# Kernel optimization log

Hardware: AMD Instinct MI355X
Metric: run time of the kernel (lower is better)

Reference implementation:

```python
import jax, jax.numpy as jnp
import numpy as np

N = 100000   # nodes
E = 1000000  # edges
IN = 100     # input feature dim
H = 4        # heads
D = 32       # hidden per head (H*D = 128)
C = 47       # classes
EPS = 1e-5
SLOPE = 0.2  # DGL GATv2 leaky_relu negative slope


def setup_inputs() -> dict:
    key = jax.random.key(0)
    ks = jax.random.split(key, 32)
    lin = lambda k, i, o: (jax.random.normal(k, (i, o), jnp.float32) / np.float32(np.sqrt(i)))
    inp = {}
    inp['x'] = jax.random.normal(ks[0], (N, IN), jnp.float32)
    inp['src'] = jax.random.randint(ks[1], (E,), 0, N, jnp.int32)
    inp['dst'] = jnp.sort(jax.random.randint(ks[2], (E,), 0, N, jnp.int32))
    # layer 0: IN -> H*D, Linear residual (IN != H*D)
    inp['Wsrc0'] = lin(ks[3], IN, H * D); inp['bsrc0'] = jnp.zeros(H * D, jnp.float32)
    inp['Wdst0'] = lin(ks[4], IN, H * D); inp['bdst0'] = jnp.zeros(H * D, jnp.float32)
    inp['attn0'] = lin(ks[5], H, D)
    inp['Wres0'] = lin(ks[6], IN, H * D); inp['bres0'] = jnp.zeros(H * D, jnp.float32)
    # layer 1: H*D -> H*D, Identity residual (128 == 128)
    inp['Wsrc1'] = lin(ks[7], H * D, H * D); inp['bsrc1'] = jnp.zeros(H * D, jnp.float32)
    inp['Wdst1'] = lin(ks[8], H * D, H * D); inp['bdst1'] = jnp.zeros(H * D, jnp.float32)
    inp['attn1'] = lin(ks[9], H, D)
    # layer 2: H*D -> H*C, Linear residual (128 != 188)
    inp['Wsrc2'] = lin(ks[10], H * D, H * C); inp['bsrc2'] = jnp.zeros(H * C, jnp.float32)
    inp['Wdst2'] = lin(ks[11], H * D, H * C); inp['bdst2'] = jnp.zeros(H * C, jnp.float32)
    inp['attn2'] = lin(ks[12], H, C)
    inp['Wres2'] = lin(ks[13], H * D, H * C); inp['bres2'] = jnp.zeros(H * C, jnp.float32)
    # BatchNorm1d params (training-mode batch stats)
    inp['g0'] = jnp.ones(H * D, jnp.float32); inp['be0'] = jnp.zeros(H * D, jnp.float32)
    inp['g1'] = jnp.ones(H * D, jnp.float32); inp['be1'] = jnp.zeros(H * D, jnp.float32)
    return inp


def _gatv2(h, src, dst, Ws, bs, Wd, bd, attn, resval):
    """One GATv2Conv on a full block (src feats == dst feats == h)."""
    Hh, Dd = attn.shape
    fs = (h @ Ws + bs).reshape(-1, Hh, Dd)   # [N,H,D] src projection
    fd = (h @ Wd + bd).reshape(-1, Hh, Dd)   # [N,H,D] dst projection
    e = jax.nn.leaky_relu(fs[src] + fd[dst], SLOPE)         # [E,H,D]
    logits = jnp.einsum('ehd,hd->eh', e, attn)              # [E,H]
    m = jax.ops.segment_max(logits, dst, num_segments=N)    # per-dst max
    ex = jnp.exp(logits - m[dst])
    s = jax.ops.segment_sum(ex, dst, num_segments=N)
    alpha = ex / s[dst]                                      # edge softmax
    out = jax.ops.segment_sum(alpha[:, :, None] * fs[src], dst, num_segments=N)
    return out + resval                                      # [N,H,D]


def _bn(x, g, b):
    mu = x.mean(0)
    v = x.var(0)  # biased, as torch BN training mode
    return g * (x - mu) / jnp.sqrt(v + EPS) + b


def reference(x, src, dst,
              Wsrc0, bsrc0, Wdst0, bdst0, attn0, Wres0, bres0,
              Wsrc1, bsrc1, Wdst1, bdst1, attn1,
              Wsrc2, bsrc2, Wdst2, bdst2, attn2, Wres2, bres2,
              g0, be0, g1, be1):
    # layer 0: conv(+relu activation) -> flatten -> BN -> relu (dropout = eval identity)
    res0 = (x @ Wres0 + bres0).reshape(N, H, D)
    h = jax.nn.relu(_gatv2(x, src, dst, Wsrc0, bsrc0, Wdst0, bdst0, attn0, res0))
    h = jax.nn.relu(_bn(h.reshape(N, H * D), g0, be0))
    # layer 1: Identity residual
    res1 = h.reshape(N, H, D)
    h = jax.nn.relu(_gatv2(h, src, dst, Wsrc1, bsrc1, Wdst1, bdst1, attn1, res1))
    h = jax.nn.relu(_bn(h.reshape(N, H * D), g1, be1))
    # layer 2: no activation; mean over heads; log_softmax
    res2 = (h @ Wres2 + bres2).reshape(N, H, C)
    h = _gatv2(h, src, dst, Wsrc2, bsrc2, Wdst2, bdst2, attn2, res2)
    h = h.mean(1)                                # [N,C]
    return jax.nn.log_softmax(h, axis=-1)
```

## Files before the change

kernel.cpp:

```cpp
#include <hip/hip_runtime.h>
#include <hip/hip_bf16.h>

#define Nn 100000
#define Ee 1000000
#define INF_ 100
#define Hh 4
#define Dd 32
#define HD 128
#define Cc 47
#define HC 188
#define HCP 192
#define EPSV 1e-5f
#define SLOPE 0.2f
#define NBLK ((Nn + 255) / 256)

typedef __hip_bfloat16 bf16;
typedef __attribute__((ext_vector_type(8))) short short8;
typedef __attribute__((ext_vector_type(4))) float f32x4;
typedef __attribute__((ext_vector_type(2))) float f32x2;

__device__ __forceinline__ float tof(bf16 v) { return __bfloat162float(v); }
__device__ __forceinline__ float b2f(unsigned short u) {
    return __uint_as_float((unsigned)u << 16);
}
__device__ __forceinline__ float ldb(const bf16* p) {
    return b2f(*(const unsigned short*)p);
}
__device__ __forceinline__ unsigned short f2u(float v) {
    bf16 t = __float2bfloat16(v);
    return *(unsigned short*)&t;
}
__device__ __forceinline__ f32x2 pk2(float x, float y) {
    f32x2 r; r.x = x; r.y = y; return r;
}
__device__ __forceinline__ f32x2 pabs2(f32x2 v) {
    return __builtin_elementwise_max(v, -v);
}
__device__ __forceinline__ f32x2 pfma2(f32x2 a, f32x2 b, f32x2 c) {
    return __builtin_elementwise_fma(a, b, c);
}

template <int C>
__device__ __forceinline__ float dppadd(float v) {
    int m = __builtin_amdgcn_update_dpp(0, __float_as_int(v), C, 0xF, 0xF, false);
    return v + __int_as_float(m);
}
template <int C>
__device__ __forceinline__ float dppmax(float v) {
    int m = __builtin_amdgcn_update_dpp(0, __float_as_int(v), C, 0xF, 0xF, false);
    return fmaxf(v, __int_as_float(m));
}
__device__ __forceinline__ float sum16(float p) {
    p = dppadd<0xB1>(p);
    p = dppadd<0x4E>(p);
    p = dppadd<0x124>(p);
    p = dppadd<0x128>(p);
    return p;
}
__device__ __forceinline__ float max16(float p) {
    p = dppmax<0xB1>(p); p = dppmax<0x4E>(p);
    p = dppmax<0x124>(p); p = dppmax<0x128>(p);
    return p;
}

#define L2E 1.4426950408889634f
#define LN2 0.6931471805599453f

__global__ void detect_dtype(const unsigned* __restrict__ x, int* __restrict__ flag) {
    if (blockIdx.x == 0 && threadIdx.x == 0) {
        int good = 0;
        for (int i = 0; i < 256; ++i) {
            unsigned lo = x[i] & 0xFFFFu;
            float v = __uint_as_float(lo << 16);
            float a = fabsf(v);
            if (a > 1e-4f && a < 10.f) good++;
        }
        *flag = (good >= 128) ? 1 : 0;
    }
}

__device__ __forceinline__ float ld_any(const void* p, int i, int isbf) {
    return isbf ? tof(((const bf16*)p)[i]) : ((const float*)p)[i];
}

__global__ void cvt_x(const void* __restrict__ in, bf16* __restrict__ out,
                      const int* __restrict__ flag) {
    int i = blockIdx.x * blockDim.x + threadIdx.x;
    if (i >= Nn * 128) return;
    int row = i >> 7, col = i & 127;
    float v = (col < INF_) ? ld_any(in, row * INF_ + col, *flag) : 0.f;
    out[i] = __float2bfloat16(v);
}

#define WROWS 1280
#define NSP 15
struct PrepTab { const void* src[8]; int row0[8]; int K[8]; int M[8]; int MP[8]; };
struct CvtTab { const void* src[NSP]; int off[NSP + 1]; };

__global__ void prep_all(PrepTab t, CvtTab ct, bf16* __restrict__ wtb,
                         bf16* __restrict__ pb, int total,
                         const int* __restrict__ flag) {
    int i = blockIdx.x * blockDim.x + threadIdx.x;
    int isbf = *flag;
    if (i < WROWS * 128) {
        int row = i >> 7, k = i & 127;
        float v = 0.f;
#pragma unroll
        for (int q = 0; q < 8; ++q) {
            if (row >= t.row0[q] && row < t.row0[q] + t.MP[q]) {
                int m = row - t.row0[q];
                if (m < t.M[q] && k < t.K[q])
                    v = ld_any(t.src[q], k * t.M[q] + m, isbf);
            }
        }
        wtb[i] = __float2bfloat16(v);
    }
    if (i < total) {
        int seg = 0;
        while (i >= ct.off[seg + 1]) seg++;
        pb[i] = __float2bfloat16(ld_any(ct.src[seg], i - ct.off[seg], isbf));
    }
}

__global__ void src_scale_ptr(const int* __restrict__ src, const int* __restrict__ dst,
                              unsigned* __restrict__ w384, unsigned* __restrict__ w256,
                              int* __restrict__ ptr,
                              float* __restrict__ z0, float* __restrict__ z1) {
    int i = blockIdx.x * blockDim.x + threadIdx.x;
    if (i < Ee) {
        unsigned s = (unsigned)src[i];
        w384[i] = s * 384u;
        w256[i] = s << 8;
    }
    if (i < 2 * HD) { z0[i] = 0.f; z1[i] = 0.f; }
    if (i <= Nn) {
        if (i == Nn) { ptr[Nn] = Ee; return; }
        int lo = 0, hi = Ee;
        while (lo < hi) {
            int mid = (lo + hi) >> 1;
            if (dst[mid] < i) lo = mid + 1; else hi = mid;
        }
        ptr[i] = lo;
    }
}

__global__ void deg_hist_blk(const int* __restrict__ ptr, int* __restrict__ cnt) {
    __shared__ int lh[256];
    int t = threadIdx.x;
    lh[t] = 0;
    __syncthreads();
    int n = blockIdx.x * 256 + t;
    if (n < Nn) {
        int dg = ptr[n + 1] - ptr[n]; if (dg > 255) dg = 255;
        atomicAdd(&lh[dg], 1);
    }
    __syncthreads();
    cnt[t * NBLK + blockIdx.x] = lh[t];
}

__global__ void deg_totals(const int* __restrict__ cnt, int* __restrict__ totals) {
    int wave = threadIdx.x >> 6, lane = threadIdx.x & 63;
    int bin = blockIdx.x * 4 + wave;
    int s = 0;
    for (int k = lane; k < NBLK; k += 64) s += cnt[bin * NBLK + k];
#pragma unroll
    for (int o = 1; o < 64; o <<= 1) s += __shfl_xor(s, o);
    if (lane == 0) totals[bin] = s;
}

__global__ void deg_bases(const int* __restrict__ cnt, const int* __restrict__ totals,
                          int* __restrict__ base) {
    int wave = threadIdx.x >> 6, lane = threadIdx.x & 63;
    int bin = blockIdx.x * 4 + wave;
    int bb = 0;
    for (int b = bin + 1 + lane; b < 256; b += 64) bb += totals[b];
#pragma unroll
    for (int o = 1; o < 64; o <<= 1) bb += __shfl_xor(bb, o);
    int run = bb;
    for (int k0 = 0; k0 < NBLK; k0 += 64) {
        int k = k0 + lane;
        int c = (k < NBLK) ? cnt[bin * NBLK + k] : 0;
        int p = c;
#pragma unroll
        for (int o = 1; o < 64; o <<= 1) {
            int t = __shfl_up(p, o);
            if (lane >= o) p += t;
        }
        if (k < NBLK) base[bin * NBLK + k] = run + (p - c);
        run += __shfl(p, 63);
    }
}

__global__ void deg_scatter_blk(const int* __restrict__ ptr, const int* __restrict__ base,
                                int* __restrict__ perm) {
    __shared__ int lh[256];
    int t = threadIdx.x;
    lh[t] = 0;
    __syncthreads();
    int n = blockIdx.x * 256 + t;
    if (n < Nn) {
        int dg = ptr[n + 1] - ptr[n]; if (dg > 255) dg = 255;
        int loc = atomicAdd(&lh[dg], 1);
        perm[base[dg * NBLK + blockIdx.x] + loc] = n;
    }
}

template <int MP, int NOUT, int CS, bool ABN, bool PAD47, int OSTR>
__global__ __launch_bounds__(256, 4) void gemm_big(
    const bf16* __restrict__ A, const bf16* __restrict__ Wt,
    const bf16* __restrict__ b0, const bf16* __restrict__ b1,
    const bf16* __restrict__ b2,
    bf16* __restrict__ o0, bf16* __restrict__ o1, bf16* __restrict__ o2,
    int MR, const float* __restrict__ bnp) {
    constexpr int CS64 = CS * 64;
    constexpr int PITCH = CS64 + 8;
    constexpr int LSZ = (64 * PITCH > 64 * 136) ? 64 * PITCH : 64 * 136;
    __shared__ __align__(16) bf16 Al[LSZ];
    const int row0 = blockIdx.x * 64;
    const int tid = threadIdx.x;
#pragma unroll
    for (int j = 0; j < 4; ++j) {
        int idx = tid + j * 256;
        int r = idx >> 4, kk = (idx & 15) * 8;
        int4 val = {0, 0, 0, 0};
        if (row0 + r < Nn) {
            val = *(const int4*)&A[(size_t)(row0 + r) * 128 + kk];
            if (ABN) {
                short8 av = *(short8*)&val;
                bf16 tmp[8];
#pragma unroll
                for (int u = 0; u < 8; ++u) {
                    float v = b2f((unsigned short)av[u]);
                    v = fmaxf(fmaf(v, bnp[kk + u], bnp[128 + kk + u]), 0.f);
                    tmp[u] = __float2bfloat16(v);
                }
                val = *(int4*)tmp;
            }
        }
        *(int4*)&Al[r * 136 + kk] = val;
    }
    __syncthreads();
    const int wave = tid >> 6, lane = tid & 63;
    const int n16 = lane & 15, quad = lane >> 4;
    const int colbase = blockIdx.y * CS64 + wave * (16 * CS);
    f32x4 acc[4][CS];
#pragma unroll
    for (int rt = 0; rt < 4; ++rt)
#pragma unroll
        for (int c = 0; c < CS; ++c) acc[rt][c] = (f32x4){0.f, 0.f, 0.f, 0.f};
    const bf16* wb[CS];
#pragma unroll
    for (int c = 0; c < CS; ++c)
        wb[c] = Wt + (size_t)(colbase + c * 16 + n16) * 128 + quad * 8;
    const bf16* ap = Al + n16 * 136 + quad * 8;
#pragma unroll
    for (int ks = 0; ks < 4; ++ks) {
        short8 bf[CS];
#pragma unroll
        for (int c = 0; c < CS; ++c) bf[c] = *(const short8*)(wb[c] + ks * 32);
#pragma unroll
        for (int rt = 0; rt < 4; ++rt) {
            short8 af = *(const short8*)(ap + rt * 16 * 136 + ks * 32);
#pragma unroll
            for (int c = 0; c < CS; ++c)
                acc[rt][c] = __builtin_amdgcn_mfma_f32_16x16x32_bf16(af, bf[c], acc[rt][c], 0, 0, 0);
        }
    }
    __syncthreads();
    if (PAD47) {
        for (int z = tid; z < 64 * PITCH; z += 256) Al[z] = __float2bfloat16(0.f);
        __syncthreads();
    }
#pragma unroll
    for (int c = 0; c < CS; ++c) {
        int pos = wave * (16 * CS) + c * 16 + n16;
        int col = colbase + c * 16 + n16;
        int oi = col / MP, lc = col - oi * MP;
        bool valid = (oi < NOUT) && (lc < MR);
        float bb = 0.f;
        if (valid) {
            const bf16* bp = (oi == 0) ? b0 : (oi == 1) ? b1 : b2;
            bb = tof(bp[lc]);
        }
        int stp = PAD47 ? (lc + lc / 47) : pos;
#pragma unroll
        for (int rt = 0; rt < 4; ++rt) {
#pragma unroll
            for (int i = 0; i < 4; ++i) {
                int rl = rt * 16 + quad * 4 + i;
                if (valid) Al[rl * PITCH + stp] = __float2bfloat16(acc[rt][c][i] + bb);
            }
        }
    }
    __syncthreads();
    constexpr int NG = CS64 / 8;
    for (int t = tid; t < 64 * NG; t += 256) {
        int rl = t / NG, g = t % NG;
        int row = row0 + rl;
        if (row >= Nn) continue;
        int pos0 = g * 8;
        int oi, lc0;
        if (PAD47) { oi = blockIdx.y; lc0 = pos0; }
        else {
            int col0 = blockIdx.y * CS64 + pos0;
            oi = col0 / MP; lc0 = col0 - oi * MP;
        }
        if (oi >= NOUT) continue;
        bf16* o = (oi == 0) ? o0 : (oi == 1) ? o1 : o2;
        int4 v = *(int4*)&Al[rl * PITCH + pos0];
        *(int4*)&o[(size_t)row * OSTR + lc0] = v;
    }
}

template <bool RESBN>
__global__ __launch_bounds__(256) void gat_fused_128(
    const bf16* __restrict__ fs, const bf16* __restrict__ fd,
    const unsigned* __restrict__ srcW, const int* __restrict__ ptr,
    const int* __restrict__ perm,
    const bf16* __restrict__ attn, const bf16* __restrict__ resb,
    const float* __restrict__ bnp, bf16* __restrict__ hout) {
    const int wave = threadIdx.x >> 6, lane = threadIdx.x & 63;
    const int di = blockIdx.x * 4 + wave;
    if (di >= Nn) return;
    const int d = perm[di];
    const int c0 = lane * 2;
    const unsigned c0b = (unsigned)c0 * 2u;
    ushort2 aq = *(const ushort2*)&attn[c0];
    float a0 = b2f(aq.x) * L2E, a1 = b2f(aq.y) * L2E;
    const f32x2 Av = pk2(0.6f * a0, 0.6f * a1);
    const f32x2 Bv = pk2(0.4f * a0, 0.4f * a1);
    ushort2 dq = *(const ushort2*)&fd[(size_t)d * HD + c0];
    const f32x2 fdv = pk2(b2f(dq.x), b2f(dq.y));
    const char* fsb = (const char*)fs;
    float l = 0.f;
    f32x2 Ov = pk2(0.f, 0.f);
    int e = ptr[d];
    const int e1 = ptr[d + 1];
    for (; e < e1 && (e & 3); ++e) {
        unsigned v = srcW[e] + c0b;
        ushort2 fq = *(const ushort2*)(fsb + v);
        f32x2 f = pk2(b2f(fq.x), b2f(fq.y));
        f32x2 x = f + fdv;
        f32x2 t = pfma2(pabs2(x), Bv, x * Av);
        float p = sum16(t.x + t.y);
        float pe = __builtin_amdgcn_exp2f(p);
        l += pe;
        Ov = pfma2(pk2(pe, pe), f, Ov);
    }
    for (; e + 3 < e1; e += 4) {
        uint4 sw = *(const uint4*)&srcW[e];
        unsigned vA = sw.x + c0b, vB = sw.y + c0b;
        unsigned vC = sw.z + c0b, vD = sw.w + c0b;
        ushort2 qA = *(const ushort2*)(fsb + vA);
        ushort2 qB = *(const ushort2*)(fsb + vB);
        ushort2 qC = *(const ushort2*)(fsb + vC);
        ushort2 qD = *(const ushort2*)(fsb + vD);
        f32x2 fA = pk2(b2f(qA.x), b2f(qA.y));
        f32x2 fB = pk2(b2f(qB.x), b2f(qB.y));
        f32x2 fC = pk2(b2f(qC.x), b2f(qC.y));
        f32x2 fD = pk2(b2f(qD.x), b2f(qD.y));
        f32x2 xA = fA + fdv, xB = fB + fdv, xC = fC + fdv, xD = fD + fdv;
        f32x2 tA = pfma2(pabs2(xA), Bv, xA * Av);
        f32x2 tB = pfma2(pabs2(xB), Bv, xB * Av);
        f32x2 tC = pfma2(pabs2(xC), Bv, xC * Av);
        f32x2 tD = pfma2(pabs2(xD), Bv, xD * Av);
        float pA = tA.x + tA.y, pB = tB.x + tB.y;
        float pC = tC.x + tC.y, pD = tD.x + tD.y;
        pA = sum16(pA); pB = sum16(pB); pC = sum16(pC); pD = sum16(pD);
        float eA = __builtin_amdgcn_exp2f(pA), eB = __builtin_amdgcn_exp2f(pB);
        float eC = __builtin_amdgcn_exp2f(pC), eD = __builtin_amdgcn_exp2f(pD);
        l += (eA + eB) + (eC + eD);
        Ov = pfma2(pk2(eA, eA), fA, Ov);
        Ov = pfma2(pk2(eB, eB), fB, Ov);
        Ov = pfma2(pk2(eC, eC), fC, Ov);
        Ov = pfma2(pk2(eD, eD), fD, Ov);
    }
    for (; e < e1; ++e) {
        unsigned v = srcW[e] + c0b;
        ushort2 fq = *(const ushort2*)(fsb + v);
        f32x2 f = pk2(b2f(fq.x), b2f(fq.y));
        f32x2 x = f + fdv;
        f32x2 t = pfma2(pabs2(x), Bv, x * Av);
        float p = sum16(t.x + t.y);
        float pe = __builtin_amdgcn_exp2f(p);
        l += pe;
        Ov = pfma2(pk2(pe, pe), f, Ov);
    }
    float inv = l > 0.f ? 1.f / l : 0.f;
    ushort2 rq = *(const ushort2*)&resb[(size_t)d * HD + c0];
    float r0 = b2f(rq.x), r1 = b2f(rq.y);
    if (RESBN) {
        r0 = fmaxf(fmaf(r0, bnp[c0], bnp[HD + c0]), 0.f);
        r1 = fmaxf(fmaf(r1, bnp[c0 + 1], bnp[HD + c0 + 1]), 0.f);
    }
    float v0 = fmaxf(fmaf(Ov.x, inv, r0), 0.f);
    float v1 = fmaxf(fmaf(Ov.y, inv, r1), 0.f);
    ushort2 ov; ov.x = f2u(v0); ov.y = f2u(v1);
    *(ushort2*)&hout[(size_t)d * HD + c0] = ov;
}

__global__ __launch_bounds__(256) void gat_fused_188(
    const bf16* __restrict__ fs, const bf16* __restrict__ fd,
    const unsigned* __restrict__ srcW, const int* __restrict__ ptr,
    const int* __restrict__ perm,
    const bf16* __restrict__ attn, const bf16* __restrict__ rs,
    void* __restrict__ out, const int* __restrict__ flag) {
    const int wave = threadIdx.x >> 6, lane = threadIdx.x & 63;
    const int di = blockIdx.x * 4 + wave;
    if (di >= Nn) return;
    const int d = perm[di];
    const int h = lane >> 4, j = lane & 15;
    const int c0 = h * 48 + j;
    const unsigned c0b = (unsigned)c0 * 2u;
    const int ca = h * Cc + j;
    const bool has2 = (j < 15);
    float a0 = ldb(&attn[ca]) * L2E;
    float a1 = ldb(&attn[ca + 16]) * L2E;
    float a2 = has2 ? ldb(&attn[ca + 32]) * L2E : 0.f;
    float A0 = 0.6f * a0, B0 = 0.4f * a0;
    float A1 = 0.6f * a1, B1 = 0.4f * a1;
    float A2 = 0.6f * a2, B2 = 0.4f * a2;
    const bf16* fdr = fd + (size_t)d * HCP;
    float fd0 = ldb(&fdr[c0]);
    float fd1 = ldb(&fdr[c0 + 16]);
    float fd2 = ldb(&fdr[c0 + 32]);
    const char* fsb = (const char*)fs;
    float l = 0.f, O0 = 0.f, O1 = 0.f, O2 = 0.f;
    int e = ptr[d];
    const int e1 = ptr[d + 1];
    for (; e + 3 < e1; e += 4) {
        unsigned vA = srcW[e] + c0b, vB = srcW[e + 1] + c0b;
        unsigned vC = srcW[e + 2] + c0b, vD = srcW[e + 3] + c0b;
        float fA0 = b2f(*(const unsigned short*)(fsb + vA));
        float fA1 = b2f(*(const unsigned short*)(fsb + vA + 32));
        float fA2 = b2f(*(const unsigned short*)(fsb + vA + 64));
        float fB0 = b2f(*(const unsigned short*)(fsb + vB));
        float fB1 = b2f(*(const unsigned short*)(fsb + vB + 32));
        float fB2 = b2f(*(const unsigned short*)(fsb + vB + 64));
        float fC0 = b2f(*(const unsigned short*)(fsb + vC));
        float fC1 = b2f(*(const unsigned short*)(fsb + vC + 32));
        float fC2 = b2f(*(const unsigned short*)(fsb + vC + 64));
        float fD0 = b2f(*(const unsigned short*)(fsb + vD));
        float fD1 = b2f(*(const unsigned short*)(fsb + vD + 32));
        float fD2 = b2f(*(const unsigned short*)(fsb + vD + 64));
        float xA0 = fA0 + fd0, xA1 = fA1 + fd1, xA2 = fA2 + fd2;
        float xB0 = fB0 + fd0, xB1 = fB1 + fd1, xB2 = fB2 + fd2;
        float xC0 = fC0 + fd0, xC1 = fC1 + fd1, xC2 = fC2 + fd2;
        float xD0 = fD0 + fd0, xD1 = fD1 + fd1, xD2 = fD2 + fd2;
        float pA = fmaf(xA0, A0, fmaf(fabsf(xA0), B0, fmaf(xA1, A1, fmaf(fabsf(xA1), B1,
                   fmaf(xA2, A2, fabsf(xA2) * B2)))));
        float pB = fmaf(xB0, A0, fmaf(fabsf(xB0), B0, fmaf(xB1, A1, fmaf(fabsf(xB1), B1,
                   fmaf(xB2, A2, fabsf(xB2) * B2)))));
        float pC = fmaf(xC0, A0, fmaf(fabsf(xC0), B0, fmaf(xC1, A1, fmaf(fabsf(xC1), B1,
                   fmaf(xC2, A2, fabsf(xC2) * B2)))));
        float pD = fmaf(xD0, A0, fmaf(fabsf(xD0), B0, fmaf(xD1, A1, fmaf(fabsf(xD1), B1,
                   fmaf(xD2, A2, fabsf(xD2) * B2)))));
        pA = sum16(pA); pB = sum16(pB); pC = sum16(pC); pD = sum16(pD);
        float eA = __builtin_amdgcn_exp2f(pA), eB = __builtin_amdgcn_exp2f(pB);
        float eC = __builtin_amdgcn_exp2f(pC), eD = __builtin_amdgcn_exp2f(pD);
        l += (eA + eB) + (eC + eD);
        O0 = fmaf(eA, fA0, O0); O0 = fmaf(eB, fB0, O0);
        O0 = fmaf(eC, fC0, O0); O0 = fmaf(eD, fD0, O0);
        O1 = fmaf(eA, fA1, O1); O1 = fmaf(eB, fB1, O1);
        O1 = fmaf(eC, fC1, O1); O1 = fmaf(eD, fD1, O1);
        O2 = fmaf(eA, fA2, O2); O2 = fmaf(eB, fB2, O2);
        O2 = fmaf(eC, fC2, O2); O2 = fmaf(eD, fD2, O2);
    }
    for (; e < e1; ++e) {
        unsigned v = srcW[e] + c0b;
        float f0 = b2f(*(const unsigned short*)(fsb + v));
        float f1 = b2f(*(const unsigned short*)(fsb + v + 32));
        float f2 = b2f(*(const unsigned short*)(fsb + v + 64));
        float x0 = f0 + fd0, x1 = f1 + fd1, x2 = f2 + fd2;
        float p = fmaf(x0, A0, fmaf(fabsf(x0), B0, fmaf(x1, A1, fmaf(fabsf(x1), B1,
                  fmaf(x2, A2, fabsf(x2) * B2)))));
        p = sum16(p);
        float pe = __builtin_amdgcn_exp2f(p);
        l += pe;
        O0 = fmaf(pe, f0, O0);
        O1 = fmaf(pe, f1, O1);
        O2 = fmaf(pe, f2, O2);
    }
    float inv = l > 0.f ? 1.f / l : 0.f;
    const bf16* rr = rs + (size_t)d * HCP;
    float v0 = fmaf(O0, inv, ldb(&rr[c0]));
    float v1 = fmaf(O1, inv, ldb(&rr[c0 + 16]));
    float v2 = has2 ? fmaf(O2, inv, ldb(&rr[c0 + 32])) : 0.f;
    v0 += __shfl_xor(v0, 16); v0 += __shfl_xor(v0, 32); v0 *= 0.25f;
    v1 += __shfl_xor(v1, 16); v1 += __shfl_xor(v1, 32); v1 *= 0.25f;
    v2 += __shfl_xor(v2, 16); v2 += __shfl_xor(v2, 32); v2 *= 0.25f;
    float mx = fmaxf(v0, v1);
    if (has2) mx = fmaxf(mx, v2);
    mx = max16(mx);
    float sm = __expf(v0 - mx) + __expf(v1 - mx) + (has2 ? __expf(v2 - mx) : 0.f);
    sm = sum16(sm);
    if (h == 0) {
        float ls = mx + __log2f(sm) * LN2;
        if (*flag) {
            bf16* o = (bf16*)out + (size_t)d * Cc;
            o[j] = __float2bfloat16(v0 - ls);
            o[j + 16] = __float2bfloat16(v1 - ls);
            if (has2) o[j + 32] = __float2bfloat16(v2 - ls);
        } else {
            float* o = (float*)out + (size_t)d * Cc;
            o[j] = v0 - ls;
            o[j + 16] = v1 - ls;
            if (has2) o[j + 32] = v2 - ls;
        }
    }
}

__global__ void col_stats(const bf16* __restrict__ in, float* __restrict__ sums) {
    int c = threadIdx.x;
    int r0 = blockIdx.x * 256;
    int r1 = r0 + 256; if (r1 > Nn) r1 = Nn;
    float s = 0.f, s2 = 0.f;
    for (int r = r0; r < r1; ++r) {
        float v = ldb(&in[(size_t)r * HD + c]);
        s += v; s2 += v * v;
    }
    atomicAdd(&sums[c], s);
    atomicAdd(&sums[HD + c], s2);
}

__global__ void bn_finalize(const float* __restrict__ sums, const bf16* __restrict__ g,
                            const bf16* __restrict__ be, float* __restrict__ ss) {
    int c = threadIdx.x;
    float mu = sums[c] * (1.f / Nn);
    float var = sums[HD + c] * (1.f / Nn) - mu * mu;
    float sc = tof(g[c]) * rsqrtf(var + EPSV);
    ss[c] = sc;
    ss[HD + c] = tof(be[c]) - mu * sc;
}

extern "C" void kernel_launch(void* const* d_in, const int* in_sizes, int n_in,
                              void* d_out, int out_size, void* d_ws, size_t ws_size,
                              hipStream_t stream) {
    (void)in_sizes; (void)n_in; (void)out_size; (void)ws_size;
    const void* x = d_in[0];
    const int* src = (const int*)d_in[1];
    const int* dst = (const int*)d_in[2];

    char* ws = (char*)d_ws;
    size_t off = 0;
    auto alloc = [&](size_t bytes) {
        void* p = ws + off;
        off += (bytes + 255) & ~(size_t)255;
        return p;
    };
    bf16* xb = (bf16*)alloc((size_t)Nn * 128 * 2);
    bf16* rb = (bf16*)alloc((size_t)Nn * HD * 2);
    bf16* rs = xb;
    bf16* fs = (bf16*)alloc((size_t)Nn * HCP * 2);
    bf16* fd = (bf16*)alloc((size_t)Nn * HCP * 2);
    bf16* hbA = (bf16*)alloc((size_t)Nn * HD * 2);
    bf16* hbB = (bf16*)alloc((size_t)Nn * HD * 2);
    int* ptr = (int*)alloc((Nn + 1) * 4);
    bf16* wtb = (bf16*)alloc((size_t)WROWS * 128 * 2);
    float* bns0 = (float*)alloc(2 * HD * 4);
    float* bns1 = (float*)alloc(2 * HD * 4);
    float* bnss0 = (float*)alloc(2 * HD * 4);
    float* bnss1 = (float*)alloc(2 * HD * 4);
    bf16* pb = (bf16*)alloc(4096 * 2);
    int* flag = (int*)alloc(256);
    unsigned* w384 = (unsigned*)alloc((size_t)Ee * 4);
    unsigned* w256 = (unsigned*)alloc((size_t)Ee * 4);
    int* cnt = (int*)alloc((size_t)256 * NBLK * 4);
    int* cbase = (int*)alloc((size_t)256 * NBLK * 4);
    int* totals = (int*)alloc(256 * 4);
    int* perm = (int*)alloc((size_t)Nn * 4);

    static const int spIdx[NSP] = {4, 6, 7, 9, 11, 13, 14, 16, 18, 19, 21, 22, 23, 24, 25};
    static const int spSz[NSP]  = {HD, HD, HD, HD, HD, HD, HD, HC, HC, HC, HC, HD, HD, HD, HD};
    CvtTab tab;
    int tot = 0;
    for (int i = 0; i < NSP; ++i) { tab.src[i] = d_in[spIdx[i]]; tab.off[i] = tot; tot += spSz[i]; }
    tab.off[NSP] = tot;
    const bf16 *bsrc0 = pb + tab.off[0], *bdst0 = pb + tab.off[1], *attn0 = pb + tab.off[2],
               *bres0 = pb + tab.off[3], *bsrc1 = pb + tab.off[4], *bdst1 = pb + tab.off[5],
               *attn1 = pb + tab.off[6], *bsrc2 = pb + tab.off[7], *bdst2 = pb + tab.off[8],
               *attn2 = pb + tab.off[9], *bres2 = pb + tab.off[10],
               *g0 = pb + tab.off[11], *be0 = pb + tab.off[12],
               *g1 = pb + tab.off[13], *be1 = pb + tab.off[14];

    PrepTab pt;
    static const int wIdx[8] = {3, 5, 8, 10, 12, 15, 17, 20};
    static const int wK[8]   = {INF_, INF_, INF_, HD, HD, HD, HD, HD};
    static const int wM[8]   = {HD, HD, HD, HD, HD, HC, HC, HC};
    static const int wMP[8]  = {128, 128, 128, 128, 128, 192, 192, 192};
    static const int wR0[8]  = {0, 128, 256, 384, 512, 640, 832, 1024};
    for (int i = 0; i < 8; ++i) {
        pt.src[i] = d_in[wIdx[i]]; pt.row0[i] = wR0[i];
        pt.K[i] = wK[i]; pt.M[i] = wM[i]; pt.MP[i] = wMP[i];
    }

    detect_dtype<<<1, 64, 0, stream>>>((const unsigned*)x, flag);
    cvt_x<<<(Nn * 128 + 255) / 256, 256, 0, stream>>>(x, xb, flag);
    prep_all<<<(WROWS * 128 + 255) / 256, 256, 0, stream>>>(pt, tab, wtb, pb, tot, flag);
    src_scale_ptr<<<(Ee + 255) / 256, 256, 0, stream>>>(src, dst, w384, w256, ptr,
                                                        bns0, bns1);
    deg_hist_blk<<<NBLK, 256, 0, stream>>>(ptr, cnt);
    deg_totals<<<64, 256, 0, stream>>>(cnt, totals);
    deg_bases<<<64, 256, 0, stream>>>(cnt, totals, cbase);
    deg_scatter_blk<<<NBLK, 256, 0, stream>>>(ptr, cbase, perm);

    const int fusedGrid = (Nn + 3) / 4;
    const int statsGrid = NBLK;
    const int rowBlk = (Nn + 63) / 64;

    gemm_big<128, 3, 3, false, false, HD><<<dim3(rowBlk, 2), 256, 0, stream>>>(
        xb, wtb, bsrc0, bdst0, bres0, fs, fd, rb, HD, nullptr);
    gat_fused_128<false><<<fusedGrid, 256, 0, stream>>>(fs, fd, w256, ptr, perm,
                                                        attn0, rb, nullptr, hbA);
    col_stats<<<statsGrid, 128, 0, stream>>>(hbA, bns0);
    bn_finalize<<<1, HD, 0, stream>>>(bns0, g0, be0, bnss0);

    gemm_big<128, 2, 2, true, false, HD><<<dim3(rowBlk, 2), 256, 0, stream>>>(
        hbA, wtb + (size_t)384 * 128, bsrc1, bdst1, nullptr, fs, fd, nullptr, HD, bnss0);
    gat_fused_128<true><<<fusedGrid, 256, 0, stream>>>(fs, fd, w256, ptr, perm,
                                                       attn1, hbA, bnss0, hbB);
    col_stats<<<statsGrid, 128, 0, stream>>>(hbB, bns1);
    bn_finalize<<<1, HD, 0, stream>>>(bns1, g1, be1, bnss1);

    gemm_big<192, 3, 3, true, true, HCP><<<dim3(rowBlk, 3), 256, 0, stream>>>(
        hbB, wtb + (size_t)640 * 128, bsrc2, bdst2, bres2, fs, fd, rs, HC, bnss1);
    gat_fused_188<<<fusedGrid, 256, 0, stream>>>(fs, fd, w384, ptr, perm, attn2, rs,
                                                 d_out, flag);
}
```

Baseline: 663.7 us.

## Fuse preprocessing kernels into one launch and fold BN finalize into consumers

Merges the dtype detection, x conversion, weight/param prep, source scaling, CSR pointer search and degree histogram into a single prepare kernel. Each block re-detects the dtype with a ballot, and the degree histogram reads CSR bounds from shared memory instead of a separate pass. The two bn_finalize launches are removed: the GEMM and gat_fused kernels compute the BN scale and offset from the raw sums themselves. This cuts about six launches and their gaps, at the cost of redundant per-thread BN math and a larger grid doing mixed work.

```diff
diff --git a/kernel.cpp b/kernel.cpp
--- a/kernel.cpp
+++ b/kernel.cpp
@@ -66,30 +66,17 @@
 #define L2E 1.4426950408889634f
 #define LN2 0.6931471805599453f
 
-__global__ void detect_dtype(const unsigned* __restrict__ x, int* __restrict__ flag) {
-    if (blockIdx.x == 0 && threadIdx.x == 0) {
-        int good = 0;
-        for (int i = 0; i < 256; ++i) {
-            unsigned lo = x[i] & 0xFFFFu;
-            float v = __uint_as_float(lo << 16);
-            float a = fabsf(v);
-            if (a > 1e-4f && a < 10.f) good++;
-        }
-        *flag = (good >= 128) ? 1 : 0;
-    }
-}
-
 __device__ __forceinline__ float ld_any(const void* p, int i, int isbf) {
     return isbf ? tof(((const bf16*)p)[i]) : ((const float*)p)[i];
 }
 
-__global__ void cvt_x(const void* __restrict__ in, bf16* __restrict__ out,
-                      const int* __restrict__ flag) {
-    int i = blockIdx.x * blockDim.x + threadIdx.x;
-    if (i >= Nn * 128) return;
-    int row = i >> 7, col = i & 127;
-    float v = (col < INF_) ? ld_any(in, row * INF_ + col, *flag) : 0.f;
-    out[i] = __float2bfloat16(v);
+__device__ __forceinline__ int lbound(const int* __restrict__ dst, int n) {
+    int lo = 0, hi = Ee;
+    while (lo < hi) {
+        int mid = (lo + hi) >> 1;
+        if (dst[mid] < n) lo = mid + 1; else hi = mid;
+    }
+    return lo;
 }
 
 #define WROWS 1280
@@ -97,65 +84,72 @@
 struct PrepTab { const void* src[8]; int row0[8]; int K[8]; int M[8]; int MP[8]; };
 struct CvtTab { const void* src[NSP]; int off[NSP + 1]; };
 
-__global__ void prep_all(PrepTab t, CvtTab ct, bf16* __restrict__ wtb,
-                         bf16* __restrict__ pb, int total,
-                         const int* __restrict__ flag) {
-    int i = blockIdx.x * blockDim.x + threadIdx.x;
-    int isbf = *flag;
-    if (i < WROWS * 128) {
-        int row = i >> 7, k = i & 127;
+__global__ __launch_bounds__(256) void prepare(
+    const void* __restrict__ x, const int* __restrict__ src,
+    const int* __restrict__ dst,
+    PrepTab pt, CvtTab ct, int tot,
+    bf16* __restrict__ xb, bf16* __restrict__ wtb, bf16* __restrict__ pb,
+    unsigned* __restrict__ w384, unsigned* __restrict__ w256,
+    int* __restrict__ ptr, int* __restrict__ cnt,
+    float* __restrict__ z0, float* __restrict__ z1, int* __restrict__ flag) {
+    __shared__ int wc[4];
+    __shared__ int lbv[257];
+    __shared__ int lh[256];
+    const int t = threadIdx.x;
+    unsigned w = ((const unsigned*)x)[t];
+    float dv = __uint_as_float((w & 0xFFFFu) << 16);
+    float da = fabsf(dv);
+    unsigned long long m = __ballot(da > 1e-4f && da < 10.f);
+    if ((t & 63) == 0) wc[t >> 6] = __popcll(m);
+    __syncthreads();
+    const int isbf = (wc[0] + wc[1] + wc[2] + wc[3]) >= 128;
+    if (blockIdx.x == 0 && t == 0) *flag = isbf;
+
+    const int gi = blockIdx.x * 256 + t;
+    if (gi < Nn * 128) {
+        int row = gi >> 7, col = gi & 127;
+        float v = (col < INF_) ? ld_any(x, row * INF_ + col, isbf) : 0.f;
+        xb[gi] = __float2bfloat16(v);
+    }
+    if (gi < WROWS * 128) {
+        int row = gi >> 7, k = gi & 127;
         float v = 0.f;
 #pragma unroll
         for (int q = 0; q < 8; ++q) {
-            if (row >= t.row0[q] && row < t.row0[q] + t.MP[q]) {
-                int m = row - t.row0[q];
-                if (m < t.M[q] && k < t.K[q])
-                    v = ld_any(t.src[q], k * t.M[q] + m, isbf);
+            if (row >= pt.row0[q] && row < pt.row0[q] + pt.MP[q]) {
+                int mm = row - pt.row0[q];
+                if (mm < pt.M[q] && k < pt.K[q])
+                    v = ld_any(pt.src[q], k * pt.M[q] + mm, isbf);
             }
         }
-        wtb[i] = __float2bfloat16(v);
-    }
-    if (i < total) {
+        wtb[gi] = __float2bfloat16(v);
+    }
+    if (gi < tot) {
         int seg = 0;
-        while (i >= ct.off[seg + 1]) seg++;
-        pb[i] = __float2bfloat16(ld_any(ct.src[seg], i - ct.off[seg], isbf));
-    }
-}
-
-__global__ void src_scale_ptr(const int* __restrict__ src, const int* __restrict__ dst,
-                              unsigned* __restrict__ w384, unsigned* __restrict__ w256,
-                              int* __restrict__ ptr,
-                              float* __restrict__ z0, float* __restrict__ z1) {
-    int i = blockIdx.x * blockDim.x + threadIdx.x;
-    if (i < Ee) {
-        unsigned s = (unsigned)src[i];
-        w384[i] = s * 384u;
-        w256[i] = s << 8;
-    }
-    if (i < 2 * HD) { z0[i] = 0.f; z1[i] = 0.f; }
-    if (i <= Nn) {
-        if (i == Nn) { ptr[Nn] = Ee; return; }
-        int lo = 0, hi = Ee;
-        while (lo < hi) {
-            int mid = (lo + hi) >> 1;
-            if (dst[mid] < i) lo = mid + 1; else hi = mid;
-        }
-        ptr[i] = lo;
-    }
-}
-
-__global__ void deg_hist_blk(const int* __restrict__ ptr, int* __restrict__ cnt) {
-    __shared__ int lh[256];
-    int t = threadIdx.x;
-    lh[t] = 0;
-    __syncthreads();
-    int n = blockIdx.x * 256 + t;
-    if (n < Nn) {
-        int dg = ptr[n + 1] - ptr[n]; if (dg > 255) dg = 255;
-        atomicAdd(&lh[dg], 1);
-    }
-    __syncthreads();
-    cnt[t * NBLK + blockIdx.x] = lh[t];
+        while (gi >= ct.off[seg + 1]) seg++;
+        pb[gi] = __float2bfloat16(ld_any(ct.src[seg], gi - ct.off[seg], isbf));
+    }
+    if (gi < Ee) {
+        unsigned s = (unsigned)src[gi];
+        w384[gi] = s * 384u;
+        w256[gi] = s << 8;
+    }
+    if (gi < 2 * HD) { z0[gi] = 0.f; z1[gi] = 0.f; }
+    if (blockIdx.x < NBLK) {
+        int nn = gi;
+        int lb = Ee;
+        if (nn <= Nn) { lb = lbound(dst, nn); ptr[nn] = lb; }
+        lbv[t] = lb;
+        if (t == 255) lbv[256] = (nn + 1 <= Nn) ? lbound(dst, nn + 1) : Ee;
+        lh[t] = 0;
+        __syncthreads();
+        if (nn < Nn) {
+            int dg = lbv[t + 1] - lbv[t]; if (dg > 255) dg = 255;
+            atomicAdd(&lh[dg], 1);
+        }
+        __syncthreads();
+        cnt[t * NBLK + blockIdx.x] = lh[t];
+    }
 }
 
 __global__ void deg_totals(const int* __restrict__ cnt, int* __restrict__ totals) {
@@ -211,13 +205,25 @@
     const bf16* __restrict__ b0, const bf16* __restrict__ b1,
     const bf16* __restrict__ b2,
     bf16* __restrict__ o0, bf16* __restrict__ o1, bf16* __restrict__ o2,
-    int MR, const float* __restrict__ bnp) {
+    int MR, const float* __restrict__ sums,
+    const bf16* __restrict__ gg, const bf16* __restrict__ bbn) {
     constexpr int CS64 = CS * 64;
     constexpr int PITCH = CS64 + 8;
     constexpr int LSZ = (64 * PITCH > 64 * 136) ? 64 * PITCH : 64 * 136;
     __shared__ __align__(16) bf16 Al[LSZ];
+    __shared__ float scb[ABN ? HD : 1], ofb[ABN ? HD : 1];
     const int row0 = blockIdx.x * 64;
     const int tid = threadIdx.x;
+    if (ABN) {
+        if (tid < HD) {
+            float mu = sums[tid] * (1.f / Nn);
+            float var = sums[HD + tid] * (1.f / Nn) - mu * mu;
+            float sc = tof(gg[tid]) * rsqrtf(var + EPSV);
+            scb[tid] = sc;
+            ofb[tid] = tof(bbn[tid]) - mu * sc;
+        }
+        __syncthreads();
+    }
 #pragma unroll
     for (int j = 0; j < 4; ++j) {
         int idx = tid + j * 256;
@@ -231,7 +237,7 @@
 #pragma unroll
                 for (int u = 0; u < 8; ++u) {
                     float v = b2f((unsigned short)av[u]);
-                    v = fmaxf(fmaf(v, bnp[kk + u], bnp[128 + kk + u]), 0.f);
+                    v = fmaxf(fmaf(v, scb[kk + u], ofb[kk + u]), 0.f);
                     tmp[u] = __float2bfloat16(v);
                 }
                 val = *(int4*)tmp;
@@ -318,7 +324,8 @@
     const unsigned* __restrict__ srcW, const int* __restrict__ ptr,
     const int* __restrict__ perm,
     const bf16* __restrict__ attn, const bf16* __restrict__ resb,
-    const float* __restrict__ bnp, bf16* __restrict__ hout) {
+    const float* __restrict__ sums, const bf16* __restrict__ gv,
+    const bf16* __restrict__ bev, bf16* __restrict__ hout) {
     const int wave = threadIdx.x >> 6, lane = threadIdx.x & 63;
     const int di = blockIdx.x * 4 + wave;
     if (di >= Nn) return;
@@ -390,8 +397,15 @@
     ushort2 rq = *(const ushort2*)&resb[(size_t)d * HD + c0];
     float r0 = b2f(rq.x), r1 = b2f(rq.y);
     if (RESBN) {
-        r0 = fmaxf(fmaf(r0, bnp[c0], bnp[HD + c0]), 0.f);
-        r1 = fmaxf(fmaf(r1, bnp[c0 + 1], bnp[HD + c0 + 1]), 0.f);
+        float mu0 = sums[c0] * (1.f / Nn), mu1 = sums[c0 + 1] * (1.f / Nn);
+        float va0 = sums[HD + c0] * (1.f / Nn) - mu0 * mu0;
+        float va1 = sums[HD + c0 + 1] * (1.f / Nn) - mu1 * mu1;
+        float sc0 = tof(gv[c0]) * rsqrtf(va0 + EPSV);
+        float sc1 = tof(gv[c0 + 1]) * rsqrtf(va1 + EPSV);
+        float of0 = tof(bev[c0]) - mu0 * sc0;
+        float of1 = tof(bev[c0 + 1]) - mu1 * sc1;
+        r0 = fmaxf(fmaf(r0, sc0, of0), 0.f);
+        r1 = fmaxf(fmaf(r1, sc1, of1), 0.f);
     }
     float v0 = fmaxf(fmaf(Ov.x, inv, r0), 0.f);
     float v1 = fmaxf(fmaf(Ov.y, inv, r1), 0.f);
@@ -523,16 +537,6 @@
     atomicAdd(&sums[HD + c], s2);
 }
 
-__global__ void bn_finalize(const float* __restrict__ sums, const bf16* __restrict__ g,
-                            const bf16* __restrict__ be, float* __restrict__ ss) {
-    int c = threadIdx.x;
-    float mu = sums[c] * (1.f / Nn);
-    float var = sums[HD + c] * (1.f / Nn) - mu * mu;
-    float sc = tof(g[c]) * rsqrtf(var + EPSV);
-    ss[c] = sc;
-    ss[HD + c] = tof(be[c]) - mu * sc;
-}
-
 extern "C" void kernel_launch(void* const* d_in, const int* in_sizes, int n_in,
                               void* d_out, int out_size, void* d_ws, size_t ws_size,
                               hipStream_t stream) {
@@ -559,8 +563,6 @@
     bf16* wtb = (bf16*)alloc((size_t)WROWS * 128 * 2);
     float* bns0 = (float*)alloc(2 * HD * 4);
     float* bns1 = (float*)alloc(2 * HD * 4);
-    float* bnss0 = (float*)alloc(2 * HD * 4);
-    float* bnss1 = (float*)alloc(2 * HD * 4);
     bf16* pb = (bf16*)alloc(4096 * 2);
     int* flag = (int*)alloc(256);
     unsigned* w384 = (unsigned*)alloc((size_t)Ee * 4);
@@ -594,12 +596,10 @@
         pt.K[i] = wK[i]; pt.M[i] = wM[i]; pt.MP[i] = wMP[i];
     }
 
-    detect_dtype<<<1, 64, 0, stream>>>((const unsigned*)x, flag);
-    cvt_x<<<(Nn * 128 + 255) / 256, 256, 0, stream>>>(x, xb, flag);
-    prep_all<<<(WROWS * 128 + 255) / 256, 256, 0, stream>>>(pt, tab, wtb, pb, tot, flag);
-    src_scale_ptr<<<(Ee + 255) / 256, 256, 0, stream>>>(src, dst, w384, w256, ptr,
-                                                        bns0, bns1);
-    deg_hist_blk<<<NBLK, 256, 0, stream>>>(ptr, cnt);
+    const int prepGrid = (Nn * 128 + 255) / 256;
+    prepare<<<prepGrid, 256, 0, stream>>>(x, src, dst, pt, tab, tot,
+                                          xb, wtb, pb, w384, w256, ptr, cnt,
+                                          bns0, bns1, flag);
     deg_totals<<<64, 256, 0, stream>>>(cnt, totals);
     deg_bases<<<64, 256, 0, stream>>>(cnt, totals, cbase);
     deg_scatter_blk<<<NBLK, 256, 0, stream>>>(ptr, cbase, perm);
@@ -609,21 +609,22 @@
     const int rowBlk = (Nn + 63) / 64;
 
     gemm_big<128, 3, 3, false, false, HD><<<dim3(rowBlk, 2), 256, 0, stream>>>(
-        xb, wtb, bsrc0, bdst0, bres0, fs, fd, rb, HD, nullptr);
+        xb, wtb, bsrc0, bdst0, bres0, fs, fd, rb, HD, nullptr, nullptr, nullptr);
     gat_fused_128<false><<<fusedGrid, 256, 0, stream>>>(fs, fd, w256, ptr, perm,
-                                                        attn0, rb, nullptr, hbA);
+                                                        attn0, rb, nullptr, nullptr,
+                                                        nullptr, hbA);
     col_stats<<<statsGrid, 128, 0, stream>>>(hbA, bns0);
-    bn_finalize<<<1, HD, 0, stream>>>(bns0, g0, be0, bnss0);
 
     gemm_big<128, 2, 2, true, false, HD><<<dim3(rowBlk, 2), 256, 0, stream>>>(
-        hbA, wtb + (size_t)384 * 128, bsrc1, bdst1, nullptr, fs, fd, nullptr, HD, bnss0);
+        hbA, wtb + (size_t)384 * 128, bsrc1, bdst1, nullptr, fs, fd, nullptr, HD,
+        bns0, g0, be0);
     gat_fused_128<true><<<fusedGrid, 256, 0, stream>>>(fs, fd, w256, ptr, perm,
-                                                       attn1, hbA, bnss0, hbB);
+                                                       attn1, hbA, bns0, g0, be0, hbB);
     col_stats<<<statsGrid, 128, 0, stream>>>(hbB, bns1);
-    bn_finalize<<<1, HD, 0, stream>>>(bns1, g1, be1, bnss1);
 
     gemm_big<192, 3, 3, true, true, HCP><<<dim3(rowBlk, 3), 256, 0, stream>>>(
-        hbB, wtb + (size_t)640 * 128, bsrc2, bdst2, bres2, fs, fd, rs, HC, bnss1);
+        hbB, wtb + (size_t)640 * 128, bsrc2, bdst2, bres2, fs, fd, rs, HC,
+        bns1, g1, be1);
     gat_fused_188<<<fusedGrid, 256, 0, stream>>>(fs, fd, w384, ptr, perm, attn2, rs,
                                                  d_out, flag);
 }
```

Result: faster. 648.7 us (-2.3%).
